# Kernel tuning notes

Hardware: AMD Instinct MI355X
Metric: run time of the kernel (lower is better)

The kernel has to match this reference:

```python
import jax, jax.numpy as jnp
import numpy as np

N_NODES = 50000
N_EDGES = 600000
N_GRAPHS = 2500
F_IN = 11  # QM9 num_node_features


def setup_inputs() -> dict:
    key = jax.random.key(0)
    ks = jax.random.split(key, 14)
    x = jax.random.normal(ks[0], (N_NODES, F_IN), jnp.float32)
    edge_index = jax.random.randint(ks[1], (2, N_EDGES), 0, N_NODES)
    batch = jnp.sort(jax.random.randint(ks[2], (N_NODES,), 0, N_GRAPHS))

    def lin(k, fan_in, fan_out):
        s = 1.0 / np.sqrt(fan_in)
        return jax.random.uniform(k, (fan_in, fan_out), jnp.float32, -s, s)

    params = dict(
        W1=lin(ks[3], F_IN, 128), b1=jnp.zeros((128,), jnp.float32),
        W2=lin(ks[4], 128, 64),   b2=jnp.zeros((64,), jnp.float32),
        Wf1=lin(ks[5], 64, 128),  bf1=jnp.zeros((128,), jnp.float32),
        Wf2=lin(ks[6], 128, 64),  bf2=jnp.zeros((64,), jnp.float32),
        Wf3=lin(ks[7], 64, 1),    bf3=jnp.zeros((1,), jnp.float32),
    )
    return dict(x=x, edge_index=edge_index, batch=batch, **params)


def reference(x, edge_index, batch, W1, b1, W2, b2, Wf1, bf1, Wf2, bf2, Wf3, bf3):
    N = x.shape[0]
    # --- GCN normalization (PyG gcn_norm): add self-loops, symmetric D^-1/2 A D^-1/2 ---
    self_loop = jnp.arange(N)
    src = jnp.concatenate([edge_index[0], self_loop])  # [E+N]
    dst = jnp.concatenate([edge_index[1], self_loop])
    deg = jax.ops.segment_sum(jnp.ones_like(dst, jnp.float32), dst, num_segments=N)
    dis = jnp.where(deg > 0, jax.lax.rsqrt(jnp.maximum(deg, 1.0)), 0.0)  # deg^-1/2
    norm = dis[src] * dis[dst]  # [E+N]

    def gcn_conv(h, W, b):
        h = h @ W  # transform first (small fan-in)
        msg = h[src] * norm[:, None]  # gather + normalize
        return jax.ops.segment_sum(msg, dst, num_segments=N) + b  # scatter-add

    h = jax.nn.relu(gcn_conv(x, W1, b1))
    h = jax.nn.relu(gcn_conv(h, W2, b2))

    # --- global_mean_pool ---
    sums = jax.ops.segment_sum(h, batch, num_segments=N_GRAPHS)
    cnt = jax.ops.segment_sum(jnp.ones((N,), jnp.float32), batch, num_segments=N_GRAPHS)
    g = sums / jnp.maximum(cnt, 1.0)[:, None]  # [G, 64]

    # --- MLP head ---
    g = jax.nn.relu(g @ Wf1 + bf1)
    g = jax.nn.relu(g @ Wf2 + bf2)
    return g @ Wf3 + bf3  # [G, 1]
```

## Files before the change

kernel.cpp:

```cpp
#include <hip/hip_runtime.h>

#define F0 11
#define F1 128
#define F2 64
#define TN 64

__global__ void k_count(const int* __restrict__ dst, int E, int* __restrict__ cnt) {
    int e = blockIdx.x * blockDim.x + threadIdx.x;
    if (e < E) atomicAdd(&cnt[dst[e]], 1);
}

__global__ void k_scanA(const int* __restrict__ deg, int* __restrict__ rowloc,
                        int* __restrict__ bsum, int N) {
    __shared__ int s[256];
    int i = blockIdx.x * 256 + threadIdx.x;
    int v = (i < N) ? deg[i] : 0;
    s[threadIdx.x] = v;
    __syncthreads();
    for (int o = 1; o < 256; o <<= 1) {
        int t = (threadIdx.x >= o) ? s[threadIdx.x - o] : 0;
        __syncthreads();
        s[threadIdx.x] += t;
        __syncthreads();
    }
    if (i < N) rowloc[i] = s[threadIdx.x] - v;
    if (threadIdx.x == 255) bsum[blockIdx.x] = s[255];
}

__global__ void k_scanB(int* __restrict__ bsum, int B) {
    __shared__ int s[256];
    int t = threadIdx.x;
    int v = (t < B) ? bsum[t] : 0;
    s[t] = v;
    __syncthreads();
    for (int o = 1; o < 256; o <<= 1) {
        int u = (t >= o) ? s[t - o] : 0;
        __syncthreads();
        s[t] += u;
        __syncthreads();
    }
    if (t < B) bsum[t] = s[t] - v;
}

__global__ void k_scanC(const int* __restrict__ rowloc, const int* __restrict__ bsum,
                        const int* __restrict__ deg, int* __restrict__ rowptr,
                        int* __restrict__ cursor, float* __restrict__ dis, int N) {
    int i = blockIdx.x * 256 + threadIdx.x;
    if (i < N) {
        int r = rowloc[i] + bsum[blockIdx.x];
        rowptr[i] = r;
        cursor[i] = r;
        dis[i] = 1.0f / sqrtf((float)(deg[i] + 1));
    }
}

__global__ void k_scatter(const int* __restrict__ src, const int* __restrict__ dst,
                          const float* __restrict__ dis, int* __restrict__ cursor,
                          int2* __restrict__ epack, int E) {
    int e = blockIdx.x * blockDim.x + threadIdx.x;
    if (e >= E) return;
    int s = src[e], d = dst[e];
    int pos = atomicAdd(&cursor[d], 1);
    epack[pos] = make_int2(s, __float_as_int(dis[s]));
}

__global__ void k_agg1l1(const int* __restrict__ rowptr, const int* __restrict__ deg,
                         const int2* __restrict__ epack, const float* __restrict__ x,
                         const float* __restrict__ dis, const float* __restrict__ W1,
                         const float* __restrict__ b1, float* __restrict__ h1, int N) {
    __shared__ float sW[F0 * F1];
    __shared__ float sb[F1];
    int t = threadIdx.x;
    for (int i = t; i < F0 * F1; i += 256) sW[i] = W1[i];
    if (t < F1) sb[t] = b1[t];
    __syncthreads();

    int wid = t >> 6, lane = t & 63;
    int n = blockIdx.x * 4 + wid;
    if (n >= N) return;

    int r0 = rowptr[n], r1 = r0 + deg[n];
    int eo = lane >> 4, f = lane & 15;

    float acc = 0.0f;
    int j = r0 + eo;
    for (; j + 4 < r1; j += 8) {
        int2 p = epack[j];
        int2 q = epack[j + 4];
        if (f < F0) {
            acc += x[p.x * F0 + f] * __int_as_float(p.y);
            acc += x[q.x * F0 + f] * __int_as_float(q.y);
        }
    }
    if (j < r1) {
        int2 p = epack[j];
        if (f < F0) acc += x[p.x * F0 + f] * __int_as_float(p.y);
    }
    acc += __shfl_xor(acc, 16, 64);
    acc += __shfl_xor(acc, 32, 64);

    float dn = dis[n];
    float afull = acc * dn;
    if (f < F0) afull += x[n * F0 + f] * dn * dn;

    float o1 = sb[lane], o2 = sb[lane + 64];
#pragma unroll
    for (int k = 0; k < F0; k++) {
        float ak = __shfl(afull, k, 64);
        o1 += ak * sW[k * F1 + lane];
        o2 += ak * sW[k * F1 + lane + 64];
    }
    h1[(size_t)n * F1 + lane]      = fmaxf(o1, 0.0f);
    h1[(size_t)n * F1 + lane + 64] = fmaxf(o2, 0.0f);
}

__global__ __launch_bounds__(256)
void k_l2gemm(const float* __restrict__ h1, const float* __restrict__ W2,
              float* __restrict__ t2, int N) {
    __shared__ float sW[F1 * F2];
    __shared__ float sHt[F1][TN + 4];
    int t = threadIdx.x;
    for (int idx = t; idx < F1 * F2 / 4; idx += 256)
        ((float4*)sW)[idx] = ((const float4*)W2)[idx];
    int n0 = blockIdx.x * TN;
    int nn = min(TN, N - n0);
    for (int idx = t; idx < nn * (F1 / 4); idx += 256) {
        int r = idx >> 5;
        int q = idx & 31;
        float4 v = ((const float4*)(h1 + (size_t)(n0 + r) * F1))[q];
        sHt[4 * q + 0][r] = v.x;
        sHt[4 * q + 1][r] = v.y;
        sHt[4 * q + 2][r] = v.z;
        sHt[4 * q + 3][r] = v.w;
    }
    __syncthreads();

    int i = t >> 4, j = t & 15;
    float4 c0 = {0,0,0,0}, c1 = {0,0,0,0}, c2 = {0,0,0,0}, c3 = {0,0,0,0};
#pragma unroll 4
    for (int k = 0; k < F1; k++) {
        float4 b = ((const float4*)(sW + k * F2))[j];
        float4 a = *(const float4*)&sHt[k][4 * i];
        c0.x += a.x * b.x; c0.y += a.x * b.y; c0.z += a.x * b.z; c0.w += a.x * b.w;
        c1.x += a.y * b.x; c1.y += a.y * b.y; c1.z += a.y * b.z; c1.w += a.y * b.w;
        c2.x += a.z * b.x; c2.y += a.z * b.y; c2.z += a.z * b.z; c2.w += a.z * b.w;
        c3.x += a.w * b.x; c3.y += a.w * b.y; c3.z += a.w * b.z; c3.w += a.w * b.w;
    }
    int nb = n0 + 4 * i;
    if (nb + 0 < N) ((float4*)(t2 + (size_t)(nb + 0) * F2))[j] = c0;
    if (nb + 1 < N) ((float4*)(t2 + (size_t)(nb + 1) * F2))[j] = c1;
    if (nb + 2 < N) ((float4*)(t2 + (size_t)(nb + 2) * F2))[j] = c2;
    if (nb + 3 < N) ((float4*)(t2 + (size_t)(nb + 3) * F2))[j] = c3;
}

__global__ void k_agg2pool(const int* __restrict__ rowptr, const int* __restrict__ deg,
                           const int2* __restrict__ epack, const float* __restrict__ t2,
                           const float* __restrict__ dis, const float* __restrict__ b2,
                           const int* __restrict__ batch, float* __restrict__ gsum,
                           float* __restrict__ gcnt, int N) {
    int t = threadIdx.x;
    int wid = t >> 6, lane = t & 63;
    int n = blockIdx.x * 4 + wid;
    if (n >= N) return;

    int r0 = rowptr[n], r1 = r0 + deg[n];
    float a0 = 0.f, a1 = 0.f, a2 = 0.f, a3 = 0.f;
    int j = r0;
    if (r1 - r0 >= 4) {
        int2 p0 = epack[j], p1 = epack[j + 1], p2 = epack[j + 2], p3 = epack[j + 3];
        float v0 = t2[(size_t)p0.x * F2 + lane];
        float v1 = t2[(size_t)p1.x * F2 + lane];
        float v2 = t2[(size_t)p2.x * F2 + lane];
        float v3 = t2[(size_t)p3.x * F2 + lane];
        j += 4;
        while (j + 4 <= r1) {
            int2 q0 = epack[j], q1 = epack[j + 1], q2 = epack[j + 2], q3 = epack[j + 3];
            float w0 = t2[(size_t)q0.x * F2 + lane];
            float w1 = t2[(size_t)q1.x * F2 + lane];
            float w2 = t2[(size_t)q2.x * F2 + lane];
            float w3 = t2[(size_t)q3.x * F2 + lane];
            a0 += __int_as_float(p0.y) * v0;
            a1 += __int_as_float(p1.y) * v1;
            a2 += __int_as_float(p2.y) * v2;
            a3 += __int_as_float(p3.y) * v3;
            p0 = q0; p1 = q1; p2 = q2; p3 = q3;
            v0 = w0; v1 = w1; v2 = w2; v3 = w3;
            j += 4;
        }
        a0 += __int_as_float(p0.y) * v0;
        a1 += __int_as_float(p1.y) * v1;
        a2 += __int_as_float(p2.y) * v2;
        a3 += __int_as_float(p3.y) * v3;
    }
    for (; j < r1; j++) {
        int2 p = epack[j];
        a0 += __int_as_float(p.y) * t2[(size_t)p.x * F2 + lane];
    }
    float acc = (a0 + a1) + (a2 + a3);
    float dn = dis[n];
    float h2 = fmaxf(acc * dn + t2[(size_t)n * F2 + lane] * dn * dn + b2[lane], 0.0f);
    int g = batch[n];
    atomicAdd(&gsum[(size_t)g * F2 + lane], h2);
    if (lane == 0) atomicAdd(&gcnt[g], 1.0f);
}

__global__ void k_head(const float* __restrict__ gsum, const float* __restrict__ gcnt,
                       const float* __restrict__ Wf1, const float* __restrict__ bf1,
                       const float* __restrict__ Wf2, const float* __restrict__ bf2,
                       const float* __restrict__ Wf3, const float* __restrict__ bf3,
                       float* __restrict__ out, int G) {
    __shared__ float sg[F2];
    __shared__ float sh1[F1];
    __shared__ float sh2[F2];
    int g = blockIdx.x, t = threadIdx.x;
    if (t < F2) {
        float c = fmaxf(gcnt[g], 1.0f);
        sg[t] = gsum[g * F2 + t] / c;
    }
    __syncthreads();
    {
        float a = bf1[t];
#pragma unroll 8
        for (int k = 0; k < F2; k++) a += sg[k] * Wf1[k * F1 + t];
        sh1[t] = fmaxf(a, 0.0f);
    }
    __syncthreads();
    if (t < F2) {
        float a = bf2[t];
#pragma unroll 8
        for (int k = 0; k < F1; k++) a += sh1[k] * Wf2[k * F2 + t];
        sh2[t] = fmaxf(a, 0.0f);
    }
    __syncthreads();
    if (t < F2) {
        float v = sh2[t] * Wf3[t];
        for (int off = 32; off > 0; off >>= 1) v += __shfl_down(v, off, 64);
        if (t == 0) out[g] = v + bf3[0];
    }
}

extern "C" void kernel_launch(void* const* d_in, const int* in_sizes, int n_in,
                              void* d_out, int out_size, void* d_ws, size_t ws_size,
                              hipStream_t stream) {
    const float* x     = (const float*)d_in[0];
    const int*   ei    = (const int*)d_in[1];
    const int*   batch = (const int*)d_in[2];
    const float* W1    = (const float*)d_in[3];
    const float* b1    = (const float*)d_in[4];
    const float* W2    = (const float*)d_in[5];
    const float* b2    = (const float*)d_in[6];
    const float* Wf1   = (const float*)d_in[7];
    const float* bf1   = (const float*)d_in[8];
    const float* Wf2   = (const float*)d_in[9];
    const float* bf2   = (const float*)d_in[10];
    const float* Wf3   = (const float*)d_in[11];
    const float* bf3   = (const float*)d_in[12];
    float* out = (float*)d_out;

    const int N = in_sizes[0] / F0;
    const int E = in_sizes[1] / 2;
    const int G = out_size;
    const int* src = ei;
    const int* dst = ei + E;

    size_t off = 0;
    auto carve = [&](size_t bytes) {
        void* p = (char*)d_ws + off;
        off += (bytes + 255) & ~(size_t)255;
        return p;
    };
    int*   deg    = (int*)  carve((size_t)N * 4);
    int*   rowloc = (int*)  carve((size_t)N * 4);
    int*   rowptr = (int*)  carve((size_t)N * 4);
    int*   cursor = (int*)  carve((size_t)N * 4);
    int*   bsum   = (int*)  carve(256 * 4);
    float* dis    = (float*)carve((size_t)N * 4);
    int2*  epack  = (int2*) carve((size_t)E * 8);
    float* h1     = (float*)carve((size_t)N * F1 * 4);
    float* t2     = (float*)carve((size_t)N * F2 * 4);
    float* gsum   = (float*)carve((size_t)G * (F2 + 1) * 4);
    float* gcnt   = gsum + (size_t)G * F2;
    (void)ws_size; (void)n_in;

    const int NB = (N + 255) / 256;

    hipMemsetAsync(deg,  0, (size_t)N * 4, stream);
    hipMemsetAsync(gsum, 0, (size_t)G * (F2 + 1) * 4, stream);

    k_count  <<<(E + 255) / 256, 256, 0, stream>>>(dst, E, deg);
    k_scanA  <<<NB, 256, 0, stream>>>(deg, rowloc, bsum, N);
    k_scanB  <<<1, 256, 0, stream>>>(bsum, NB);
    k_scanC  <<<NB, 256, 0, stream>>>(rowloc, bsum, deg, rowptr, cursor, dis, N);
    k_scatter<<<(E + 255) / 256, 256, 0, stream>>>(src, dst, dis, cursor, epack, E);
    k_agg1l1 <<<(N + 3) / 4, 256, 0, stream>>>(rowptr, deg, epack, x, dis, W1, b1, h1, N);
    k_l2gemm <<<(N + TN - 1) / TN, 256, 0, stream>>>(h1, W2, t2, N);
    k_agg2pool<<<(N + 3) / 4, 256, 0, stream>>>(rowptr, deg, epack, t2, dis, b2, batch, gsum, gcnt, N);
    k_head   <<<G, F1, 0, stream>>>(gsum, gcnt, Wf1, bf1, Wf2, bf2, Wf3, bf3, out, G);
}
```

Baseline: 269.0 us.

## Fuse CSR build stages into one cooperative kernel with grid syncs

```diff
diff --git a/kernel.cpp b/kernel.cpp
--- a/kernel.cpp
+++ b/kernel.cpp
@@ -1,67 +1,80 @@
 #include <hip/hip_runtime.h>
+#include <hip/hip_cooperative_groups.h>
+
+namespace cg = cooperative_groups;
 
 #define F0 11
 #define F1 128
 #define F2 64
 #define TN 64
 
-__global__ void k_count(const int* __restrict__ dst, int E, int* __restrict__ cnt) {
-    int e = blockIdx.x * blockDim.x + threadIdx.x;
-    if (e < E) atomicAdd(&cnt[dst[e]], 1);
-}
-
-__global__ void k_scanA(const int* __restrict__ deg, int* __restrict__ rowloc,
-                        int* __restrict__ bsum, int N) {
+__global__ void k_build(const int* __restrict__ src, const int* __restrict__ dst,
+                        int E, int N, int G,
+                        int* __restrict__ deg, int* __restrict__ bsum,
+                        int* __restrict__ rowptr, int* __restrict__ cursor,
+                        float* __restrict__ dis, int2* __restrict__ epack,
+                        float* __restrict__ gsum) {
+    cg::grid_group grid = cg::this_grid();
     __shared__ int s[256];
-    int i = blockIdx.x * 256 + threadIdx.x;
-    int v = (i < N) ? deg[i] : 0;
-    s[threadIdx.x] = v;
-    __syncthreads();
-    for (int o = 1; o < 256; o <<= 1) {
-        int t = (threadIdx.x >= o) ? s[threadIdx.x - o] : 0;
+    const int t   = threadIdx.x;
+    const int c   = blockIdx.x;
+    const int tid = c * 256 + t;
+    const int nth = gridDim.x * 256;
+    const int nchunk = (N + 255) >> 8;
+
+    for (int i = tid; i < N; i += nth) deg[i] = 0;
+    for (int i = tid; i < G * (F2 + 1); i += nth) gsum[i] = 0.0f;
+    grid.sync();
+
+    for (int e = tid; e < E; e += nth) atomicAdd(&deg[dst[e]], 1);
+    grid.sync();
+
+    if (c < nchunk) {
+        int i = c * 256 + t;
+        int v = (i < N) ? deg[i] : 0;
+        s[t] = v;
         __syncthreads();
-        s[threadIdx.x] += t;
+        for (int o = 1; o < 256; o <<= 1) {
+            int u = (t >= o) ? s[t - o] : 0;
+            __syncthreads();
+            s[t] += u;
+            __syncthreads();
+        }
+        if (i < N) rowptr[i] = s[t] - v;
+        if (t == 255) bsum[c] = s[255];
+    }
+    grid.sync();
+
+    if (c == 0) {
+        int v = (t < nchunk) ? bsum[t] : 0;
+        s[t] = v;
         __syncthreads();
-    }
-    if (i < N) rowloc[i] = s[threadIdx.x] - v;
-    if (threadIdx.x == 255) bsum[blockIdx.x] = s[255];
-}
-
-__global__ void k_scanB(int* __restrict__ bsum, int B) {
-    __shared__ int s[256];
-    int t = threadIdx.x;
-    int v = (t < B) ? bsum[t] : 0;
-    s[t] = v;
-    __syncthreads();
-    for (int o = 1; o < 256; o <<= 1) {
-        int u = (t >= o) ? s[t - o] : 0;
-        __syncthreads();
-        s[t] += u;
-        __syncthreads();
-    }
-    if (t < B) bsum[t] = s[t] - v;
-}
-
-__global__ void k_scanC(const int* __restrict__ rowloc, const int* __restrict__ bsum,
-                        const int* __restrict__ deg, int* __restrict__ rowptr,
-                        int* __restrict__ cursor, float* __restrict__ dis, int N) {
-    int i = blockIdx.x * 256 + threadIdx.x;
-    if (i < N) {
-        int r = rowloc[i] + bsum[blockIdx.x];
-        rowptr[i] = r;
-        cursor[i] = r;
-        dis[i] = 1.0f / sqrtf((float)(deg[i] + 1));
-    }
-}
-
-__global__ void k_scatter(const int* __restrict__ src, const int* __restrict__ dst,
-                          const float* __restrict__ dis, int* __restrict__ cursor,
-                          int2* __restrict__ epack, int E) {
-    int e = blockIdx.x * blockDim.x + threadIdx.x;
-    if (e >= E) return;
-    int s = src[e], d = dst[e];
-    int pos = atomicAdd(&cursor[d], 1);
-    epack[pos] = make_int2(s, __float_as_int(dis[s]));
+        for (int o = 1; o < 256; o <<= 1) {
+            int u = (t >= o) ? s[t - o] : 0;
+            __syncthreads();
+            s[t] += u;
+            __syncthreads();
+        }
+        if (t < nchunk) bsum[t] = s[t] - v;
+    }
+    grid.sync();
+
+    if (c < nchunk) {
+        int i = c * 256 + t;
+        if (i < N) {
+            int r = rowptr[i] + bsum[c];
+            rowptr[i] = r;
+            cursor[i] = r;
+            dis[i] = 1.0f / sqrtf((float)(deg[i] + 1));
+        }
+    }
+    grid.sync();
+
+    for (int e = tid; e < E; e += nth) {
+        int sn = src[e], d = dst[e];
+        int pos = atomicAdd(&cursor[d], 1);
+        epack[pos] = make_int2(sn, __float_as_int(dis[sn]));
+    }
 }
 
 __global__ void k_agg1l1(const int* __restrict__ rowptr, const int* __restrict__ deg,
@@ -257,9 +270,9 @@
     const float* bf3   = (const float*)d_in[12];
     float* out = (float*)d_out;
 
-    const int N = in_sizes[0] / F0;
-    const int E = in_sizes[1] / 2;
-    const int G = out_size;
+    int N = in_sizes[0] / F0;
+    int E = in_sizes[1] / 2;
+    int G = out_size;
     const int* src = ei;
     const int* dst = ei + E;
 
@@ -270,7 +283,6 @@
         return p;
     };
     int*   deg    = (int*)  carve((size_t)N * 4);
-    int*   rowloc = (int*)  carve((size_t)N * 4);
     int*   rowptr = (int*)  carve((size_t)N * 4);
     int*   cursor = (int*)  carve((size_t)N * 4);
     int*   bsum   = (int*)  carve(256 * 4);
@@ -282,16 +294,11 @@
     float* gcnt   = gsum + (size_t)G * F2;
     (void)ws_size; (void)n_in;
 
-    const int NB = (N + 255) / 256;
-
-    hipMemsetAsync(deg,  0, (size_t)N * 4, stream);
-    hipMemsetAsync(gsum, 0, (size_t)G * (F2 + 1) * 4, stream);
-
-    k_count  <<<(E + 255) / 256, 256, 0, stream>>>(dst, E, deg);
-    k_scanA  <<<NB, 256, 0, stream>>>(deg, rowloc, bsum, N);
-    k_scanB  <<<1, 256, 0, stream>>>(bsum, NB);
-    k_scanC  <<<NB, 256, 0, stream>>>(rowloc, bsum, deg, rowptr, cursor, dis, N);
-    k_scatter<<<(E + 255) / 256, 256, 0, stream>>>(src, dst, dis, cursor, epack, E);
+    void* kargs[] = { (void*)&src, (void*)&dst, (void*)&E, (void*)&N, (void*)&G,
+                      (void*)&deg, (void*)&bsum, (void*)&rowptr, (void*)&cursor,
+                      (void*)&dis, (void*)&epack, (void*)&gsum };
+    hipLaunchCooperativeKernel((void*)k_build, dim3(1024), dim3(256), kargs, 0, stream);
+
     k_agg1l1 <<<(N + 3) / 4, 256, 0, stream>>>(rowptr, deg, epack, x, dis, W1, b1, h1, N);
     k_l2gemm <<<(N + TN - 1) / TN, 256, 0, stream>>>(h1, W2, t2, N);
     k_agg2pool<<<(N + 3) / 4, 256, 0, stream>>>(rowptr, deg, epack, t2, dis, b2, batch, gsum, gcnt, N);
```

New measurement: 747.8 us. 178% more time.

## Fuse layer-1 aggregation with layer-2 GEMM via shared-memory tile, drop h1 buffer

Applied to the files above, without the earlier changes.

```diff
diff --git a/kernel.cpp b/kernel.cpp
--- a/kernel.cpp
+++ b/kernel.cpp
@@ -64,74 +64,70 @@
     epack[pos] = make_int2(s, __float_as_int(dis[s]));
 }
 
-__global__ void k_agg1l1(const int* __restrict__ rowptr, const int* __restrict__ deg,
-                         const int2* __restrict__ epack, const float* __restrict__ x,
-                         const float* __restrict__ dis, const float* __restrict__ W1,
-                         const float* __restrict__ b1, float* __restrict__ h1, int N) {
-    __shared__ float sW[F0 * F1];
-    __shared__ float sb[F1];
+__global__ __launch_bounds__(256)
+void k_agg1l2(const int* __restrict__ rowptr, const int* __restrict__ deg,
+              const int2* __restrict__ epack, const float* __restrict__ x,
+              const float* __restrict__ dis, const float* __restrict__ W1,
+              const float* __restrict__ b1, const float* __restrict__ W2,
+              float* __restrict__ t2, float* __restrict__ gz, int zlen, int N) {
+    __shared__ float sW2[F1 * F2];
+    __shared__ float sHt[F1][TN + 4];
+    __shared__ float sW1[F0 * F1];
+    __shared__ float sb1[F1];
     int t = threadIdx.x;
-    for (int i = t; i < F0 * F1; i += 256) sW[i] = W1[i];
-    if (t < F1) sb[t] = b1[t];
+
+    {
+        int per = (zlen + gridDim.x - 1) / gridDim.x;
+        int s0 = blockIdx.x * per;
+        int s1 = min(s0 + per, zlen);
+        for (int i = s0 + t; i < s1; i += 256) gz[i] = 0.0f;
+    }
+    for (int i = t; i < F1 * F2 / 4; i += 256)
+        ((float4*)sW2)[i] = ((const float4*)W2)[i];
+    for (int i = t; i < F0 * F1; i += 256) sW1[i] = W1[i];
+    if (t < F1) sb1[t] = b1[t];
     __syncthreads();
 
     int wid = t >> 6, lane = t & 63;
-    int n = blockIdx.x * 4 + wid;
-    if (n >= N) return;
-
-    int r0 = rowptr[n], r1 = r0 + deg[n];
+    int n0 = blockIdx.x * TN;
     int eo = lane >> 4, f = lane & 15;
 
-    float acc = 0.0f;
-    int j = r0 + eo;
-    for (; j + 4 < r1; j += 8) {
-        int2 p = epack[j];
-        int2 q = epack[j + 4];
-        if (f < F0) {
-            acc += x[p.x * F0 + f] * __int_as_float(p.y);
-            acc += x[q.x * F0 + f] * __int_as_float(q.y);
+    for (int c = 0; c < 16; c++) {
+        int ln = wid * 16 + c;
+        int n = n0 + ln;
+        if (n < N) {
+            int r0 = rowptr[n], r1 = r0 + deg[n];
+            float acc = 0.0f;
+            int j = r0 + eo;
+            for (; j + 4 < r1; j += 8) {
+                int2 p = epack[j];
+                int2 q = epack[j + 4];
+                if (f < F0) {
+                    acc += x[p.x * F0 + f] * __int_as_float(p.y);
+                    acc += x[q.x * F0 + f] * __int_as_float(q.y);
+                }
+            }
+            if (j < r1) {
+                int2 p = epack[j];
+                if (f < F0) acc += x[p.x * F0 + f] * __int_as_float(p.y);
+            }
+            acc += __shfl_xor(acc, 16, 64);
+            acc += __shfl_xor(acc, 32, 64);
+
+            float dn = dis[n];
+            float afull = acc * dn;
+            if (f < F0) afull += x[n * F0 + f] * dn * dn;
+
+            float o1 = sb1[lane], o2 = sb1[lane + 64];
+#pragma unroll
+            for (int k = 0; k < F0; k++) {
+                float ak = __shfl(afull, k, 64);
+                o1 += ak * sW1[k * F1 + lane];
+                o2 += ak * sW1[k * F1 + lane + 64];
+            }
+            sHt[lane][ln]      = fmaxf(o1, 0.0f);
+            sHt[lane + 64][ln] = fmaxf(o2, 0.0f);
         }
-    }
-    if (j < r1) {
-        int2 p = epack[j];
-        if (f < F0) acc += x[p.x * F0 + f] * __int_as_float(p.y);
-    }
-    acc += __shfl_xor(acc, 16, 64);
-    acc += __shfl_xor(acc, 32, 64);
-
-    float dn = dis[n];
-    float afull = acc * dn;
-    if (f < F0) afull += x[n * F0 + f] * dn * dn;
-
-    float o1 = sb[lane], o2 = sb[lane + 64];
-#pragma unroll
-    for (int k = 0; k < F0; k++) {
-        float ak = __shfl(afull, k, 64);
-        o1 += ak * sW[k * F1 + lane];
-        o2 += ak * sW[k * F1 + lane + 64];
-    }
-    h1[(size_t)n * F1 + lane]      = fmaxf(o1, 0.0f);
-    h1[(size_t)n * F1 + lane + 64] = fmaxf(o2, 0.0f);
-}
-
-__global__ __launch_bounds__(256)
-void k_l2gemm(const float* __restrict__ h1, const float* __restrict__ W2,
-              float* __restrict__ t2, int N) {
-    __shared__ float sW[F1 * F2];
-    __shared__ float sHt[F1][TN + 4];
-    int t = threadIdx.x;
-    for (int idx = t; idx < F1 * F2 / 4; idx += 256)
-        ((float4*)sW)[idx] = ((const float4*)W2)[idx];
-    int n0 = blockIdx.x * TN;
-    int nn = min(TN, N - n0);
-    for (int idx = t; idx < nn * (F1 / 4); idx += 256) {
-        int r = idx >> 5;
-        int q = idx & 31;
-        float4 v = ((const float4*)(h1 + (size_t)(n0 + r) * F1))[q];
-        sHt[4 * q + 0][r] = v.x;
-        sHt[4 * q + 1][r] = v.y;
-        sHt[4 * q + 2][r] = v.z;
-        sHt[4 * q + 3][r] = v.w;
     }
     __syncthreads();
 
@@ -139,7 +135,7 @@
     float4 c0 = {0,0,0,0}, c1 = {0,0,0,0}, c2 = {0,0,0,0}, c3 = {0,0,0,0};
 #pragma unroll 4
     for (int k = 0; k < F1; k++) {
-        float4 b = ((const float4*)(sW + k * F2))[j];
+        float4 b = ((const float4*)(sW2 + k * F2))[j];
         float4 a = *(const float4*)&sHt[k][4 * i];
         c0.x += a.x * b.x; c0.y += a.x * b.y; c0.z += a.x * b.z; c0.w += a.x * b.w;
         c1.x += a.y * b.x; c1.y += a.y * b.y; c1.z += a.y * b.z; c1.w += a.y * b.w;
@@ -276,24 +272,23 @@
     int*   bsum   = (int*)  carve(256 * 4);
     float* dis    = (float*)carve((size_t)N * 4);
     int2*  epack  = (int2*) carve((size_t)E * 8);
-    float* h1     = (float*)carve((size_t)N * F1 * 4);
     float* t2     = (float*)carve((size_t)N * F2 * 4);
     float* gsum   = (float*)carve((size_t)G * (F2 + 1) * 4);
     float* gcnt   = gsum + (size_t)G * F2;
     (void)ws_size; (void)n_in;
 
     const int NB = (N + 255) / 256;
-
-    hipMemsetAsync(deg,  0, (size_t)N * 4, stream);
-    hipMemsetAsync(gsum, 0, (size_t)G * (F2 + 1) * 4, stream);
+    const int zlen = G * (F2 + 1);
+
+    hipMemsetAsync(deg, 0, (size_t)N * 4, stream);
 
     k_count  <<<(E + 255) / 256, 256, 0, stream>>>(dst, E, deg);
     k_scanA  <<<NB, 256, 0, stream>>>(deg, rowloc, bsum, N);
     k_scanB  <<<1, 256, 0, stream>>>(bsum, NB);
     k_scanC  <<<NB, 256, 0, stream>>>(rowloc, bsum, deg, rowptr, cursor, dis, N);
     k_scatter<<<(E + 255) / 256, 256, 0, stream>>>(src, dst, dis, cursor, epack, E);
-    k_agg1l1 <<<(N + 3) / 4, 256, 0, stream>>>(rowptr, deg, epack, x, dis, W1, b1, h1, N);
-    k_l2gemm <<<(N + TN - 1) / TN, 256, 0, stream>>>(h1, W2, t2, N);
+    k_agg1l2 <<<(N + TN - 1) / TN, 256, 0, stream>>>(rowptr, deg, epack, x, dis,
+                                                     W1, b1, W2, t2, gsum, zlen, N);
     k_agg2pool<<<(N + 3) / 4, 256, 0, stream>>>(rowptr, deg, epack, t2, dis, b2, batch, gsum, gcnt, N);
     k_head   <<<G, F1, 0, stream>>>(gsum, gcnt, Wf1, bf1, Wf2, bf2, Wf3, bf3, out, G);
 }
```

Measured after the change: 295.1 us. 1.1x slower.
